# Kernel optimization log

Measured on AMD Instinct MI355X. Metric: run time of the kernel, lower is better.

Reference implementation:

```python
import jax, jax.numpy as jnp
import numpy as np

N_GRID = 512
B = 4
NUM_VIEWS = 4
EPS = 1e-6


def _build_mesh(n):
    # grid mesh with |v| in (0, 0.9] so log(|v|/(1-|v|)) is finite and sign(v) != 0
    xs = np.linspace(-0.9, 0.9, n, dtype=np.float32)  # 512 points -> no exact zero
    X, Y = np.meshgrid(xs, xs, indexing='ij')
    Z = 0.1 * np.abs(np.sin(3.0 * X) * np.cos(3.0 * Y)) + 0.01
    V = np.stack([X, Y, Z], -1).reshape(-1, 3).astype(np.float32)
    idx = np.arange(n * n).reshape(n, n)
    v00, v01 = idx[:-1, :-1].ravel(), idx[:-1, 1:].ravel()
    v10, v11 = idx[1:, :-1].ravel(), idx[1:, 1:].ravel()
    f1 = np.stack([v00, v10, v01], -1)
    f2 = np.stack([v10, v11, v01], -1)
    F = np.concatenate([f1, f2], 0).astype(np.int64)
    return V, F


def _topology(F, nv):
    # per-face edges + the opposite vertex of each edge within its face
    e = np.concatenate([F[:, [0, 1]], F[:, [1, 2]], F[:, [2, 0]]], 0)
    opp = np.concatenate([F[:, 2], F[:, 0], F[:, 1]], 0)
    key = np.sort(e, axis=1)
    uniq, inv, counts = np.unique(key, axis=0, return_inverse=True, return_counts=True)
    # LaplacianLoss: unique neighbor pairs (matrix assignment dedups), both directions
    src = np.concatenate([uniq[:, 0], uniq[:, 1]]).astype(np.int32)
    dst = np.concatenate([uniq[:, 1], uniq[:, 0]]).astype(np.int32)
    deg = np.bincount(dst, minlength=nv).astype(np.int32)
    # FlattenLoss: edges shared by exactly two faces -> (v0,v1) edge, (v2,v3) opposite verts
    order = np.argsort(inv, kind='stable')
    starts = np.searchsorted(inv[order], np.arange(len(uniq)))
    m2 = counts == 2
    i1 = order[starts[m2]]
    i2 = order[starts[m2] + 1]
    v0s = uniq[m2, 0].astype(np.int32)
    v1s = uniq[m2, 1].astype(np.int32)
    v2s = opp[i1].astype(np.int32)
    v3s = opp[i2].astype(np.int32)
    return src, dst, deg, v0s, v1s, v2s, v3s


def setup_inputs() -> dict:
    key = jax.random.key(0)
    k1, k2, k3 = jax.random.split(key, 3)
    Vt, F = _build_mesh(N_GRID)
    nv = Vt.shape[0]
    src, dst, deg, v0s, v1s, v2s, v3s = _topology(F, nv)
    return {
        'displace': jax.random.normal(k1, (B, nv, 3), jnp.float32) * 0.1,
        'center': jax.random.normal(k2, (B, 1, 3), jnp.float32) * 0.1,
        'texture': jax.random.uniform(k3, (B, nv, 3), jnp.float32),
        'template_vertices': jnp.asarray(Vt)[None],  # [1, V, 3]
        'lap_src': jnp.asarray(src),
        'lap_dst': jnp.asarray(dst),
        'deg': jnp.asarray(deg),
        'v0s': jnp.asarray(v0s),
        'v1s': jnp.asarray(v1s),
        'v2s': jnp.asarray(v2s),
        'v3s': jnp.asarray(v3s),
        'num_views': NUM_VIEWS,
    }


def reference(displace, center, texture, template_vertices, lap_src, lap_dst, deg,
              v0s, v1s, v2s, v3s, num_views):
    nv = template_vertices.shape[1]
    tv = template_vertices  # [1, V, 3]
    # vertex warp (elementwise)
    base = jnp.log(jnp.abs(tv) / (1.0 - jnp.abs(tv)))
    centroid = jnp.tanh(center)  # [B, 1, 3]
    v = jax.nn.sigmoid(base + displace) * jnp.sign(tv)  # [B, V, 3]
    v = jax.nn.relu(v) * (1.0 - centroid) - jax.nn.relu(-v) * (centroid + 1.0)
    v = v + centroid

    # uniform Laplacian loss: Lx = x - mean(neighbors); sum of squares per batch, mean over batch
    inv_deg = 1.0 / deg.astype(v.dtype)

    def lap_one(x):  # x: [V, 3]
        nbr = jax.ops.segment_sum(x[lap_src], lap_dst, num_segments=nv)
        return x - nbr * inv_deg[:, None]

    lx = jax.vmap(lap_one)(v)
    lap_loss = jnp.mean(jnp.sum(lx * lx, axis=(1, 2)))

    # flatten loss over face pairs sharing an edge
    p0, p1, p2, p3 = v[:, v0s], v[:, v1s], v[:, v2s], v[:, v3s]  # [B, P, 3]
    a1 = p1 - p0
    a1l2 = jnp.sum(a1 * a1, -1)
    a1l1 = jnp.sqrt(a1l2 + EPS)

    def _comp(b):
        bl2 = jnp.sum(b * b, -1)
        bl1 = jnp.sqrt(bl2 + EPS)
        ab = jnp.sum(a1 * b, -1)
        cos = ab / (a1l1 * bl1 + EPS)
        sin = jnp.sqrt(1.0 - cos * cos + EPS)
        cb = b - a1 * (ab / (a1l2 + EPS))[..., None]
        return cb, bl1 * sin

    cb1, l1 = _comp(p2 - p0)
    cb2, l2 = _comp(p3 - p0)
    cos = jnp.sum(cb1 * cb2, -1) / (l1 * l2 + EPS)
    flat_loss = jnp.mean(jnp.sum((cos + 1.0) ** 2, axis=1))

    # torch repeat(1, numViews, 1).reshape(numViews*B, V, 3) == tile then reshape
    b = v.shape[0]
    verts_out = jnp.tile(v, (1, num_views, 1)).reshape(num_views * b, nv, 3)
    tex_out = jnp.tile(texture, (1, num_views, 1)).reshape(num_views * b, nv, 3)
    return verts_out, tex_out, lap_loss, flat_loss
```

## Files before the change

kernel.cpp:

```cpp
#include <hip/hip_runtime.h>

#define NGRID 512
#define NV (NGRID * NGRID)
#define NB 4
#define NVIEWS 4
#define FEPS 1e-6f
#define TR 2
#define LDS_ROWS (TR + 2)
#define ROWF (NGRID * 3)
#define LDSF4 (LDS_ROWS * ROWF / 4)

typedef float fvec4 __attribute__((ext_vector_type(4)));

static constexpr size_t NVF3 = (size_t)NV * 3;
static constexpr size_t VERTS_FLOATS = (size_t)NVIEWS * NB * NVF3;
static constexpr size_t LAP_OFF = 2 * VERTS_FLOATS;
static constexpr size_t FLAT_OFF = LAP_OFF + 1;

__device__ __forceinline__ float frcp(float x)  { return __builtin_amdgcn_rcpf(x); }
__device__ __forceinline__ float fsqrt_(float x){ return __builtin_amdgcn_sqrtf(x); }

__global__ void init_losses(float* __restrict__ out) {
    if (threadIdx.x == 0) {
        out[LAP_OFF] = 0.0f;
        out[FLAT_OFF] = 0.0f;
    }
}

__device__ __forceinline__ float edge_val(fvec4 p0, fvec4 p1, fvec4 p2, fvec4 p3) {
    const float a1x = p1.x - p0.x, a1y = p1.y - p0.y, a1z = p1.z - p0.z;
    const float a1l2 = a1x * a1x + a1y * a1y + a1z * a1z;
    const float a1l1 = fsqrt_(a1l2 + FEPS);
    const float inv_a1l2 = frcp(a1l2 + FEPS);

    const float b1x = p2.x - p0.x, b1y = p2.y - p0.y, b1z = p2.z - p0.z;
    const float b1l2 = b1x * b1x + b1y * b1y + b1z * b1z;
    const float b1l1 = fsqrt_(b1l2 + FEPS);
    const float ab1 = a1x * b1x + a1y * b1y + a1z * b1z;
    const float cos1 = ab1 * frcp(a1l1 * b1l1 + FEPS);
    const float sin1 = fsqrt_(1.0f - cos1 * cos1 + FEPS);
    const float f1 = ab1 * inv_a1l2;
    const float cb1x = b1x - a1x * f1, cb1y = b1y - a1y * f1, cb1z = b1z - a1z * f1;
    const float l1 = b1l1 * sin1;

    const float b2x = p3.x - p0.x, b2y = p3.y - p0.y, b2z = p3.z - p0.z;
    const float b2l2 = b2x * b2x + b2y * b2y + b2z * b2z;
    const float b2l1 = fsqrt_(b2l2 + FEPS);
    const float ab2 = a1x * b2x + a1y * b2y + a1z * b2z;
    const float cos2 = ab2 * frcp(a1l1 * b2l1 + FEPS);
    const float sin2 = fsqrt_(1.0f - cos2 * cos2 + FEPS);
    const float f2 = ab2 * inv_a1l2;
    const float cb2x = b2x - a1x * f2, cb2y = b2y - a1y * f2, cb2z = b2z - a1z * f2;
    const float l2 = b2l1 * sin2;

    const float cosd = (cb1x * cb2x + cb1y * cb2y + cb1z * cb2z) * frcp(l1 * l2 + FEPS);
    const float t = cosd + 1.0f;
    return t * t;
}

__global__ __launch_bounds__(256, 4) void mesh_fused_kernel(
    const float* __restrict__ disp, const float* __restrict__ center,
    const float* __restrict__ tex, const float* __restrict__ tv,
    float* __restrict__ out)
{
    __shared__ fvec4 vsp[LDS_ROWS * NGRID + 1];
    float* __restrict__ vs_f = (float*)vsp;

    const int tid = threadIdx.x;
    const int b = blockIdx.y;
    const int R0 = blockIdx.x * TR;

    const float c0 = tanhf(center[b * 3 + 0]);
    const float c1 = tanhf(center[b * 3 + 1]);
    const float c2 = tanhf(center[b * 3 + 2]);
    const float carr[3] = {c0, c1, c2};

    {
        const fvec4* __restrict__ tv4 = (const fvec4*)tv;
        const fvec4* __restrict__ d4p = (const fvec4*)(disp + (size_t)b * NVF3);
        const fvec4* __restrict__ t4p = (const fvec4*)(tex + (size_t)b * NVF3);
        fvec4* __restrict__ out4 = (fvec4*)out;
        const size_t blk4 = NVF3 / 4;
        const int start4 = (R0 - 1) * (ROWF / 4);
#pragma unroll
        for (int ss = 0; ss < LDSF4 / 256; ++ss) {
            const int q = ss * 256 + tid;
            const int g4 = start4 + q;
            const int rowq = q / (ROWF / 4);
            if (g4 >= 0 && g4 < (int)(NVF3 / 4)) {
                const fvec4 t = tv4[g4];
                const fvec4 d = d4p[g4];
                fvec4 vr;
                int comp = q % 3;
#pragma unroll
                for (int l = 0; l < 4; ++l) {
                    const float tvl = t[l];
                    const float s = fabsf(tvl);
                    const float sgn = (tvl > 0.0f) ? 1.0f : -1.0f;
                    const float e = __expf(-d[l]);
                    const float sigma = s * frcp(fmaf(1.0f - s, e, s));
                    const float c = carr[comp];
                    vr[l] = fmaf(sigma, sgn - c, c);
                    comp = (comp == 2) ? 0 : comp + 1;
                }
                {
                    const int k = q / 3;
                    const int cc = q - 3 * k;
                    int point = 4 * k + cc;
                    int comp2 = cc;
#pragma unroll
                    for (int l = 0; l < 4; ++l) {
                        vs_f[point * 4 + comp2] = vr[l];
                        comp2++;
                        if (comp2 == 3) { comp2 = 0; point++; }
                    }
                }
                if (rowq >= 1 && rowq <= TR) {
                    const fvec4 tx = __builtin_nontemporal_load(&t4p[g4]);
#pragma unroll
                    for (int view = 0; view < NVIEWS; ++view) {
                        const size_t base = (size_t)(b * NVIEWS + view) * blk4;
                        __builtin_nontemporal_store(vr, &out4[base + g4]);
                        __builtin_nontemporal_store(tx, &out4[(VERTS_FLOATS / 4) + base + g4]);
                    }
                }
            }
        }
    }
    __syncthreads();

    float lap_sum = 0.0f, flat_sum = 0.0f;
#pragma unroll 1
    for (int it = 0; it < TR * NGRID / 256; ++it) {
        const int idx = it * 256 + tid;
        const int r_off = idx >> 9;
        const int c = idx & (NGRID - 1);
        const int gr = R0 + r_off;
        const int lr = r_off + 1;
        const int base = lr * NGRID + c;

        const fvec4 C  = vsp[base];
        const fvec4 Nn = vsp[base - NGRID];
        const fvec4 S  = vsp[base + NGRID];
        const fvec4 W  = vsp[base - 1];
        const fvec4 E  = vsp[base + 1];
        const fvec4 NE = vsp[base - NGRID + 1];
        const fvec4 SW = vsp[base + NGRID - 1];
        const fvec4 SE = vsp[base + NGRID + 1];

        {
            float sx = 0.f, sy = 0.f, sz = 0.f;
            int deg = 0;
            if (gr > 0)               { sx += Nn.x; sy += Nn.y; sz += Nn.z; deg++; }
            if (gr < NGRID - 1)       { sx += S.x;  sy += S.y;  sz += S.z;  deg++; }
            if (c > 0)                { sx += W.x;  sy += W.y;  sz += W.z;  deg++; }
            if (c < NGRID - 1)        { sx += E.x;  sy += E.y;  sz += E.z;  deg++; }
            if (gr > 0 && c < NGRID - 1)      { sx += NE.x; sy += NE.y; sz += NE.z; deg++; }
            if (gr < NGRID - 1 && c > 0)      { sx += SW.x; sy += SW.y; sz += SW.z; deg++; }
            const float id = frcp((float)deg);
            const float lx = C.x - sx * id;
            const float ly = C.y - sy * id;
            const float lz = C.z - sz * id;
            lap_sum += lx * lx + ly * ly + lz * lz;
        }

        if (gr < NGRID - 1 && c < NGRID - 1) {
            flat_sum += edge_val(E, S, C, SE);
        }
        if (gr >= 1 && gr < NGRID - 1 && c < NGRID - 1) {
            flat_sum += edge_val(C, E, S, NE);
        }
        if (gr < NGRID - 1 && c >= 1 && c < NGRID - 1) {
            flat_sum += edge_val(C, S, E, SW);
        }
    }

#pragma unroll
    for (int off = 32; off > 0; off >>= 1) {
        lap_sum  += __shfl_down(lap_sum, off, 64);
        flat_sum += __shfl_down(flat_sum, off, 64);
    }
    __shared__ float red[8];
    const int lane = tid & 63;
    const int wid = tid >> 6;
    if (lane == 0) { red[wid] = lap_sum; red[4 + wid] = flat_sum; }
    __syncthreads();
    if (tid == 0) {
        const float ls = red[0] + red[1] + red[2] + red[3];
        const float fs = red[4] + red[5] + red[6] + red[7];
        atomicAdd(&out[LAP_OFF],  ls * (1.0f / NB));
        atomicAdd(&out[FLAT_OFF], fs * (1.0f / NB));
    }
}

extern "C" void kernel_launch(void* const* d_in, const int* in_sizes, int n_in,
                              void* d_out, int out_size, void* d_ws, size_t ws_size,
                              hipStream_t stream)
{
    const float* disp   = (const float*)d_in[0];
    const float* center = (const float*)d_in[1];
    const float* tex    = (const float*)d_in[2];
    const float* tv     = (const float*)d_in[3];
    float* out = (float*)d_out;

    init_losses<<<1, 64, 0, stream>>>(out);
    mesh_fused_kernel<<<dim3(NGRID / TR, NB), 256, 0, stream>>>(disp, center, tex, tv, out);
}
```

Measured before the change: 187.0 us.

## Pad LDS rows, move output writes after barrier, register-tile stencil strips

Each LDS row is padded to 640 slots with a per-4-column skew to cut bank conflicts on the scattered float stores and the stencil reads. The replicated vertex and texture writes now run after the barrier, reading vertices back from LDS, and use ordinary stores instead of nontemporal ones. The stencil loop is restructured so each thread loads a 3x6 register tile once and processes four adjacent columns, reusing neighbours instead of reloading eight vectors per vertex. The min-occupancy launch bound is dropped, which lets register use grow and may lower occupancy for this memory-bound kernel.

After: 176.1 us. -5.8%, faster.

```diff
diff --git a/kernel.cpp b/kernel.cpp
--- a/kernel.cpp
+++ b/kernel.cpp
@@ -9,6 +9,7 @@
 #define LDS_ROWS (TR + 2)
 #define ROWF (NGRID * 3)
 #define LDSF4 (LDS_ROWS * ROWF / 4)
+#define SROW 640
 
 typedef float fvec4 __attribute__((ext_vector_type(4)));
 
@@ -58,40 +59,37 @@
     return t * t;
 }
 
-__global__ __launch_bounds__(256, 4) void mesh_fused_kernel(
+__global__ __launch_bounds__(256) void mesh_fused_kernel(
     const float* __restrict__ disp, const float* __restrict__ center,
     const float* __restrict__ tex, const float* __restrict__ tv,
     float* __restrict__ out)
 {
-    __shared__ fvec4 vsp[LDS_ROWS * NGRID + 1];
+    __shared__ fvec4 vsp[LDS_ROWS * SROW];
     float* __restrict__ vs_f = (float*)vsp;
 
     const int tid = threadIdx.x;
     const int b = blockIdx.y;
     const int R0 = blockIdx.x * TR;
 
-    const float c0 = tanhf(center[b * 3 + 0]);
-    const float c1 = tanhf(center[b * 3 + 1]);
-    const float c2 = tanhf(center[b * 3 + 2]);
-    const float carr[3] = {c0, c1, c2};
+    const float c0c = tanhf(center[b * 3 + 0]);
+    const float c1c = tanhf(center[b * 3 + 1]);
+    const float c2c = tanhf(center[b * 3 + 2]);
+    const float carr[3] = {c0c, c1c, c2c};
 
     {
         const fvec4* __restrict__ tv4 = (const fvec4*)tv;
         const fvec4* __restrict__ d4p = (const fvec4*)(disp + (size_t)b * NVF3);
-        const fvec4* __restrict__ t4p = (const fvec4*)(tex + (size_t)b * NVF3);
-        fvec4* __restrict__ out4 = (fvec4*)out;
-        const size_t blk4 = NVF3 / 4;
         const int start4 = (R0 - 1) * (ROWF / 4);
 #pragma unroll
         for (int ss = 0; ss < LDSF4 / 256; ++ss) {
-            const int q = ss * 256 + tid;
-            const int g4 = start4 + q;
-            const int rowq = q / (ROWF / 4);
-            if (g4 >= 0 && g4 < (int)(NVF3 / 4)) {
-                const fvec4 t = tv4[g4];
-                const fvec4 d = d4p[g4];
-                fvec4 vr;
-                int comp = q % 3;
+            const int ff4 = ss * 256 + tid;
+            const int g4 = start4 + ff4;
+            if (g4 < 0 || g4 >= (int)(NVF3 / 4)) continue;
+            const fvec4 t = tv4[g4];
+            const fvec4 d = d4p[g4];
+            fvec4 vr;
+            {
+                int comp = ff4 % 3;
 #pragma unroll
                 for (int l = 0; l < 4; ++l) {
                     const float tvl = t[l];
@@ -103,75 +101,122 @@
                     vr[l] = fmaf(sigma, sgn - c, c);
                     comp = (comp == 2) ? 0 : comp + 1;
                 }
-                {
-                    const int k = q / 3;
-                    const int cc = q - 3 * k;
-                    int point = 4 * k + cc;
-                    int comp2 = cc;
-#pragma unroll
-                    for (int l = 0; l < 4; ++l) {
-                        vs_f[point * 4 + comp2] = vr[l];
-                        comp2++;
-                        if (comp2 == 3) { comp2 = 0; point++; }
-                    }
+            }
+            {
+                const int k = ff4 / 3;
+                const int m = ff4 - 3 * k;
+                int point = 4 * k + m;
+                int comp = m;
+#pragma unroll
+                for (int l = 0; l < 4; ++l) {
+                    const int row = point >> 9;
+                    const int col = point & (NGRID - 1);
+                    const int slot = row * SROW + col + (col >> 2);
+                    vs_f[slot * 4 + comp] = vr[l];
+                    comp++;
+                    if (comp == 3) { comp = 0; point++; }
                 }
-                if (rowq >= 1 && rowq <= TR) {
-                    const fvec4 tx = __builtin_nontemporal_load(&t4p[g4]);
-#pragma unroll
-                    for (int view = 0; view < NVIEWS; ++view) {
-                        const size_t base = (size_t)(b * NVIEWS + view) * blk4;
-                        __builtin_nontemporal_store(vr, &out4[base + g4]);
-                        __builtin_nontemporal_store(tx, &out4[(VERTS_FLOATS / 4) + base + g4]);
-                    }
+            }
+        }
+    }
+    __syncthreads();
+
+    {
+        const fvec4* __restrict__ t4p = (const fvec4*)(tex + (size_t)b * NVF3);
+        fvec4* __restrict__ out4 = (fvec4*)out;
+        const size_t blk4 = NVF3 / 4;
+        const int tile_base4 = R0 * (ROWF / 4);
+#pragma unroll
+        for (int qq = 0; qq < TR * ROWF / 4 / 256; ++qq) {
+            const int q = qq * 256 + tid;
+            fvec4 vo;
+            {
+                const int qt = (ROWF / 4) + q;
+                const int k = qt / 3;
+                const int m = qt - 3 * k;
+                int point = 4 * k + m;
+                int comp = m;
+#pragma unroll
+                for (int l = 0; l < 4; ++l) {
+                    const int row = point >> 9;
+                    const int col = point & (NGRID - 1);
+                    const int slot = row * SROW + col + (col >> 2);
+                    vo[l] = vs_f[slot * 4 + comp];
+                    comp++;
+                    if (comp == 3) { comp = 0; point++; }
                 }
             }
-        }
-    }
-    __syncthreads();
+            const fvec4 tx = t4p[tile_base4 + q];
+            const size_t pos4 = (size_t)tile_base4 + q;
+#pragma unroll
+            for (int view = 0; view < NVIEWS; ++view) {
+                const size_t base = (size_t)(b * NVIEWS + view) * blk4;
+                out4[base + pos4] = vo;
+                out4[(VERTS_FLOATS / 4) + base + pos4] = tx;
+            }
+        }
+    }
 
     float lap_sum = 0.0f, flat_sum = 0.0f;
-#pragma unroll 1
-    for (int it = 0; it < TR * NGRID / 256; ++it) {
-        const int idx = it * 256 + tid;
-        const int r_off = idx >> 9;
-        const int c = idx & (NGRID - 1);
-        const int gr = R0 + r_off;
-        const int lr = r_off + 1;
-        const int base = lr * NGRID + c;
-
-        const fvec4 C  = vsp[base];
-        const fvec4 Nn = vsp[base - NGRID];
-        const fvec4 S  = vsp[base + NGRID];
-        const fvec4 W  = vsp[base - 1];
-        const fvec4 E  = vsp[base + 1];
-        const fvec4 NE = vsp[base - NGRID + 1];
-        const fvec4 SW = vsp[base + NGRID - 1];
-        const fvec4 SE = vsp[base + NGRID + 1];
-
-        {
-            float sx = 0.f, sy = 0.f, sz = 0.f;
-            int deg = 0;
-            if (gr > 0)               { sx += Nn.x; sy += Nn.y; sz += Nn.z; deg++; }
-            if (gr < NGRID - 1)       { sx += S.x;  sy += S.y;  sz += S.z;  deg++; }
-            if (c > 0)                { sx += W.x;  sy += W.y;  sz += W.z;  deg++; }
-            if (c < NGRID - 1)        { sx += E.x;  sy += E.y;  sz += E.z;  deg++; }
-            if (gr > 0 && c < NGRID - 1)      { sx += NE.x; sy += NE.y; sz += NE.z; deg++; }
-            if (gr < NGRID - 1 && c > 0)      { sx += SW.x; sy += SW.y; sz += SW.z; deg++; }
-            const float id = frcp((float)deg);
-            const float lx = C.x - sx * id;
-            const float ly = C.y - sy * id;
-            const float lz = C.z - sz * id;
-            lap_sum += lx * lx + ly * ly + lz * lz;
-        }
-
-        if (gr < NGRID - 1 && c < NGRID - 1) {
-            flat_sum += edge_val(E, S, C, SE);
-        }
-        if (gr >= 1 && gr < NGRID - 1 && c < NGRID - 1) {
-            flat_sum += edge_val(C, E, S, NE);
-        }
-        if (gr < NGRID - 1 && c >= 1 && c < NGRID - 1) {
-            flat_sum += edge_val(C, S, E, SW);
+    {
+        const int rofs = tid >> 7;
+        const int strip = tid & 127;
+        const int cb = strip * 4;
+        const int gr = R0 + rofs;
+        const int lr = rofs + 1;
+
+        const int cm1 = (cb > 0) ? cb - 1 : 0;
+        const int cp4 = (cb + 4 < NGRID) ? cb + 4 : NGRID - 1;
+        const int cols[6] = {cm1, cb, cb + 1, cb + 2, cb + 3, cp4};
+
+        fvec4 P[3][6];
+#pragma unroll
+        for (int r = 0; r < 3; ++r) {
+            const int rbase = (lr - 1 + r) * SROW;
+#pragma unroll
+            for (int kk = 0; kk < 6; ++kk) {
+                const int cc = cols[kk];
+                P[r][kk] = vsp[rbase + cc + (cc >> 2)];
+            }
+        }
+
+#pragma unroll
+        for (int j = 0; j < 4; ++j) {
+            const int c = cb + j;
+            const fvec4 C  = P[1][j + 1];
+            const fvec4 Nn = P[0][j + 1];
+            const fvec4 S  = P[2][j + 1];
+            const fvec4 W  = P[1][j];
+            const fvec4 E  = P[1][j + 2];
+            const fvec4 NE = P[0][j + 2];
+            const fvec4 SW = P[2][j];
+            const fvec4 SE = P[2][j + 2];
+
+            {
+                float sx = 0.f, sy = 0.f, sz = 0.f;
+                int deg = 0;
+                if (gr > 0)               { sx += Nn.x; sy += Nn.y; sz += Nn.z; deg++; }
+                if (gr < NGRID - 1)       { sx += S.x;  sy += S.y;  sz += S.z;  deg++; }
+                if (c > 0)                { sx += W.x;  sy += W.y;  sz += W.z;  deg++; }
+                if (c < NGRID - 1)        { sx += E.x;  sy += E.y;  sz += E.z;  deg++; }
+                if (gr > 0 && c < NGRID - 1)      { sx += NE.x; sy += NE.y; sz += NE.z; deg++; }
+                if (gr < NGRID - 1 && c > 0)      { sx += SW.x; sy += SW.y; sz += SW.z; deg++; }
+                const float id = frcp((float)deg);
+                const float lx = C.x - sx * id;
+                const float ly = C.y - sy * id;
+                const float lz = C.z - sz * id;
+                lap_sum += lx * lx + ly * ly + lz * lz;
+            }
+
+            if (gr < NGRID - 1 && c < NGRID - 1) {
+                flat_sum += edge_val(E, S, C, SE);
+            }
+            if (gr >= 1 && gr < NGRID - 1 && c < NGRID - 1) {
+                flat_sum += edge_val(C, E, S, NE);
+            }
+            if (gr < NGRID - 1 && c >= 1 && c < NGRID - 1) {
+                flat_sum += edge_val(C, S, E, SW);
+            }
         }
     }
 
```
